# Performance work log

Hardware: AMD Instinct MI355X
Metric: run time of the kernel (lower is better)

Reference implementation:

```python
import jax, jax.numpy as jnp
import numpy as np

H = 8          # num_heads
SCALE = 25.0   # attention temperature
THRESH = 0.75  # raw cosine-similarity mask threshold


def _l2n(x):
    return x / jnp.linalg.norm(x, axis=-1, keepdims=True)


def setup_inputs() -> dict:
    key = jax.random.key(0)
    ks = jax.random.split(key, 8)
    B, N, C, OUT = 1, 2048, 1024, 1024
    s = 0.02
    return {
        "x_cls": jax.random.normal(ks[0], (B, N, C), jnp.float32),
        "x_reg": jax.random.normal(ks[1], (B, N, C), jnp.float32),
        "cls_score": jax.random.uniform(ks[2], (N,), jnp.float32),
        "fg_score": jax.random.uniform(ks[3], (N,), jnp.float32),
        "W_qkv_cls": jax.random.normal(ks[4], (3 * C, C), jnp.float32) * s,
        "W_qkv_reg": jax.random.normal(ks[5], (3 * C, C), jnp.float32) * s,
        "W1": jax.random.normal(ks[6], (2 * C, 2 * C), jnp.float32) * s,
        "b1": jnp.zeros((2 * C,), jnp.float32),
        "W2": jax.random.normal(ks[7], (OUT, 4 * C), jnp.float32) * s,
        "b2": jnp.zeros((OUT,), jnp.float32),
    }


def reference(x_cls, x_reg, cls_score, fg_score, W_qkv_cls, W_qkv_reg, W1, b1, W2, b2):
    B, N, C = x_cls.shape
    d = C // H

    def split_qkv(x, W):
        # nn.Linear (no bias): x @ W.T, then [B,N,3,H,d] -> [3,B,H,N,d]
        qkv = (x @ W.T).reshape(B, N, 3, H, d).transpose(2, 0, 3, 1, 4)
        return qkv[0], qkv[1], qkv[2]

    q_cls, k_cls, v_cls = split_qkv(x_cls, W_qkv_cls)
    q_reg, k_reg, _ = split_qkv(x_reg, W_qkv_reg)

    q_cls, k_cls = _l2n(q_cls), _l2n(k_cls)
    q_reg, k_reg = _l2n(q_reg), _l2n(k_reg)
    v_cls_n = _l2n(v_cls)

    cs = cls_score.reshape(1, 1, 1, N)  # broadcast over [B,H,N,N]
    fs = fg_score.reshape(1, 1, 1, N)

    attn_cls_raw = jnp.einsum('bhnd,bhmd->bhnm', v_cls_n, v_cls_n)
    attn_cls = jax.nn.softmax(jnp.einsum('bhnd,bhmd->bhnm', q_cls, k_cls) * SCALE * cs, axis=-1)
    attn_reg = jax.nn.softmax(jnp.einsum('bhnd,bhmd->bhnm', q_reg, k_reg) * SCALE * fs, axis=-1)
    attn = (attn_reg + attn_cls) * 0.5

    x = jnp.einsum('bhnm,bhmd->bhnd', attn, v_cls).transpose(0, 2, 1, 3).reshape(B, N, C)
    x_ori = v_cls.transpose(0, 2, 1, 3).reshape(B, N, C)
    trans_cls = jnp.concatenate([x, x_ori], axis=-1)  # [B,N,2C]

    # head-averaged similarity, masked and re-normalized (batch element 0)
    sim_raw = attn_cls_raw.sum(axis=1)[0] / H          # [N,N]
    sim_mask = (sim_raw > THRESH).astype(x_cls.dtype)
    sim_attn = attn.sum(axis=1)[0] / H
    sim_round2 = jax.nn.softmax(sim_attn, axis=-1)
    masked = sim_mask * sim_round2
    sim_round2 = masked / masked.sum(axis=-1, keepdims=True)

    msa = trans_cls @ W1.T + b1                        # linear1 [B,N,2C]
    feat = msa[0]                                      # [N,2C]
    soft_sim = sim_round2 @ feat                       # [N,2C]
    ave = jnp.concatenate([soft_sim, feat], axis=-1)   # [N,4C]
    out = ave @ W2.T + b2                              # [N,OUT]
    return out
```

## Files before the change

### kernel.cpp

```cpp
#include <hip/hip_runtime.h>
#include <math.h>

#define PN 2048
#define PC 1024
#define PH 8
#define PD 128
#define PC3 3072

typedef __bf16 bf16x8 __attribute__((ext_vector_type(8)));
typedef float  f32x4  __attribute__((ext_vector_type(4)));
typedef short  s8v    __attribute__((ext_vector_type(8)));
typedef short  s4v    __attribute__((ext_vector_type(4)));

__device__ __forceinline__ short f2bf(float x) {
    unsigned u = __float_as_uint(x);
    unsigned r = (u + 0x7fffu + ((u >> 16) & 1u)) >> 16;
    return (short)r;
}
__device__ __forceinline__ float bf2f(short s) {
    return __uint_as_float(((unsigned)(unsigned short)s) << 16);
}

#define LDS_DMA(g, l) __builtin_amdgcn_global_load_lds( \
    (const __attribute__((address_space(1))) void*)(g), \
    (__attribute__((address_space(3))) void*)(l), 16, 0, 0)

__device__ __forceinline__ void stage128(const short* g, long ld, short* lds,
                                         int wave, int lrow, int lcol)
{
#pragma unroll
    for (int kc = 0; kc < 4; ++kc) {
        LDS_DMA(g + (long)lrow * ld + kc * 32 + lcol, lds + kc * 4096 + wave * 512);
        LDS_DMA(g + (long)(lrow + 64) * ld + kc * 32 + lcol,
                lds + kc * 4096 + 2048 + wave * 512);
    }
}

template<int BN, bool OBF16, bool BIAS>
__global__ __launch_bounds__(256) void mfma_gemm_k(
    const short* __restrict__ A, int lda, long zsa,
    const short* __restrict__ B, int ldb, long zsb,
    void* __restrict__ Cv, int ldc, long zsc,
    int K, float alpha, const float* __restrict__ bias)
{
    constexpr int NJ = BN / 32;
    __shared__ short As[128 * 32];
    __shared__ short Bs[BN * 32];
    const int tid = threadIdx.x;
    const int wave = tid >> 6, lane = tid & 63;
    const int lrow = tid >> 2;
    const int lcol = (tid & 3) * 8;
    const int z = blockIdx.z;
    A += (long)z * zsa;
    B += (long)z * zsb;
    const int row0 = blockIdx.y * 128, col0 = blockIdx.x * BN;
    const short* Ag = A + (long)(row0 + lrow) * lda + lcol;
    const short* Bg = B + (long)(col0 + lrow) * ldb + lcol;
    short* AsW0 = As + wave * 512;
    short* AsW1 = As + 2048 + wave * 512;
    short* BsW0 = Bs + wave * 512;
    short* BsW1 = Bs + 2048 + wave * 512;
    const int wr = (wave >> 1) * 64, wc = (wave & 1) * (BN / 2);
    const int m16 = lane & 15, q8 = (lane >> 4) * 8;

    f32x4 acc[4][NJ];
#pragma unroll
    for (int i = 0; i < 4; ++i)
#pragma unroll
        for (int j = 0; j < NJ; ++j) acc[i][j] = (f32x4){0.f, 0.f, 0.f, 0.f};

    for (int kt = 0; kt < K; kt += 32) {
        if (kt) __syncthreads();
        LDS_DMA(Ag + kt, AsW0);
        LDS_DMA(Ag + kt + 64 * (long)lda, AsW1);
        LDS_DMA(Bg + kt, BsW0);
        if (BN == 128) LDS_DMA(Bg + kt + 64 * (long)ldb, BsW1);
        __syncthreads();
        bf16x8 a[4], b[NJ];
#pragma unroll
        for (int i = 0; i < 4; ++i)
            a[i] = *(const bf16x8*)&As[(wr + i * 16 + m16) * 32 + q8];
#pragma unroll
        for (int j = 0; j < NJ; ++j)
            b[j] = *(const bf16x8*)&Bs[(wc + j * 16 + m16) * 32 + q8];
#pragma unroll
        for (int i = 0; i < 4; ++i)
#pragma unroll
            for (int j = 0; j < NJ; ++j)
                acc[i][j] = __builtin_amdgcn_mfma_f32_16x16x32_bf16(a[i], b[j], acc[i][j], 0, 0, 0);
    }

    const long cz = (long)z * zsc;
#pragma unroll
    for (int i = 0; i < 4; ++i) {
        const int r0 = row0 + wr + i * 16 + (lane >> 4) * 4;
#pragma unroll
        for (int j = 0; j < NJ; ++j) {
            const int c = col0 + wc + j * 16 + m16;
            const float bv = BIAS ? bias[c] : 0.0f;
#pragma unroll
            for (int t = 0; t < 4; ++t) {
                const float x = acc[i][j][t] * alpha + bv;
                const long off = cz + (long)(r0 + t) * ldc + c;
                if (OBF16) ((short*)Cv)[off] = f2bf(x);
                else       ((float*)Cv)[off] = x;
            }
        }
    }
}

__global__ __launch_bounds__(256) void attn_rowsum_k(
    const short* __restrict__ qkv,
    const float* __restrict__ cls_score, const float* __restrict__ fg_score,
    float* __restrict__ l_g)
{
    __shared__ short Qs[16384];
    __shared__ short Ks[16384];
    __shared__ float lsum[128][2];
    const int tid = threadIdx.x, wave = tid >> 6, lane = tid & 63;
    const int lrow = tid >> 2, lcol = (tid & 3) * 8;
    const int wr = (wave >> 1) * 64, wc = (wave & 1) * 64;
    const int m16 = lane & 15, q4 = lane >> 4, q8 = q4 * 8;
    const int row0 = blockIdx.x * 128, h = blockIdx.y, side = blockIdx.z;
    const float* sc_g = side ? fg_score : cls_score;
    const short* base = qkv + (long)side * PN * PC3 + h * PD;
    const short* Kg = base + PC;
    stage128(base + (long)row0 * PC3, PC3, Qs, wave, lrow, lcol);
    stage128(Kg, PC3, Ks, wave, lrow, lcol);
    __syncthreads();
    bf16x8 a[4][4];
#pragma unroll
    for (int i = 0; i < 4; ++i)
#pragma unroll
        for (int kc = 0; kc < 4; ++kc)
            a[i][kc] = *(const bf16x8*)&Qs[kc * 4096 + (wr + i * 16 + m16) * 32 + q8];
    float rs[4][4] = {};
    for (int ct = 0; ct < 16; ++ct) {
        if (ct) {
            __syncthreads();
            stage128(Kg + (long)ct * 128 * PC3, PC3, Ks, wave, lrow, lcol);
            __syncthreads();
        }
        f32x4 acc[4][4];
#pragma unroll
        for (int i = 0; i < 4; ++i)
#pragma unroll
            for (int j = 0; j < 4; ++j) acc[i][j] = (f32x4){0.f, 0.f, 0.f, 0.f};
#pragma unroll
        for (int kc = 0; kc < 4; ++kc) {
            bf16x8 b[4];
#pragma unroll
            for (int j = 0; j < 4; ++j)
                b[j] = *(const bf16x8*)&Ks[kc * 4096 + (wc + j * 16 + m16) * 32 + q8];
#pragma unroll
            for (int i = 0; i < 4; ++i)
#pragma unroll
                for (int j = 0; j < 4; ++j)
                    acc[i][j] = __builtin_amdgcn_mfma_f32_16x16x32_bf16(a[i][kc], b[j], acc[i][j], 0, 0, 0);
        }
#pragma unroll
        for (int j = 0; j < 4; ++j) {
            const float s25 = 25.0f * sc_g[ct * 128 + wc + j * 16 + m16];
#pragma unroll
            for (int i = 0; i < 4; ++i)
#pragma unroll
                for (int t = 0; t < 4; ++t)
                    rs[i][t] += __expf(acc[i][j][t] * s25);
        }
    }
#pragma unroll
    for (int i = 0; i < 4; ++i)
#pragma unroll
        for (int t = 0; t < 4; ++t) {
            float v = rs[i][t];
            v += __shfl_xor(v, 1, 64); v += __shfl_xor(v, 2, 64);
            v += __shfl_xor(v, 4, 64); v += __shfl_xor(v, 8, 64);
            if (m16 == 0) lsum[wr + i * 16 + q4 * 4 + t][wave & 1] = v;
        }
    __syncthreads();
    if (tid < 128)
        l_g[((long)side * PH + h) * PN + row0 + tid] = lsum[tid][0] + lsum[tid][1];
}

__global__ __launch_bounds__(256) void attn_combine_k(
    const short* __restrict__ qkv,
    const float* __restrict__ cls_score, const float* __restrict__ fg_score,
    const float* __restrict__ l_g,
    short* __restrict__ attn8, float* __restrict__ sim_attn)
{
    __shared__ short Ts[32768];
    const int tid = threadIdx.x, wave = tid >> 6, lane = tid & 63;
    const int lrow = tid >> 2, lcol = (tid & 3) * 8;
    const int wr = (wave >> 1) * 64, wc = (wave & 1) * 64;
    const int m16 = lane & 15, q4 = lane >> 4, q8 = q4 * 8;
    const int col0 = blockIdx.x * 128, row0 = blockIdx.y * 128;
    const long NN = (long)PN * PN;

    f32x4 sim[4][4];
#pragma unroll
    for (int i = 0; i < 4; ++i)
#pragma unroll
        for (int j = 0; j < 4; ++j) sim[i][j] = (f32x4){0.f, 0.f, 0.f, 0.f};
    f32x4 comb[4][4];

    for (int st = 0; st < 16; ++st) {
        const int h = st >> 1, s = st & 1;
        const short* bq = qkv + (long)s * PN * PC3 + h * PD;
        __syncthreads();
        stage128(bq + (long)row0 * PC3, PC3, Ts, wave, lrow, lcol);
        stage128(bq + PC + (long)col0 * PC3, PC3, Ts + 16384, wave, lrow, lcol);
        __syncthreads();

        float rl[4];
#pragma unroll
        for (int j = 0; j < 4; ++j)
            rl[j] = 0.5f / l_g[((long)s * PH + h) * PN + row0 + wr + j * 16 + m16];

        f32x4 acc[4][4];
#pragma unroll
        for (int i = 0; i < 4; ++i)
#pragma unroll
            for (int j = 0; j < 4; ++j) acc[i][j] = (f32x4){0.f, 0.f, 0.f, 0.f};
#pragma unroll
        for (int kc = 0; kc < 4; ++kc) {
            bf16x8 kf[4], qf[4];
#pragma unroll
            for (int i = 0; i < 4; ++i)
                kf[i] = *(const bf16x8*)&Ts[16384 + kc * 4096 + (wc + i * 16 + m16) * 32 + q8];
#pragma unroll
            for (int j = 0; j < 4; ++j)
                qf[j] = *(const bf16x8*)&Ts[kc * 4096 + (wr + j * 16 + m16) * 32 + q8];
#pragma unroll
            for (int i = 0; i < 4; ++i)
#pragma unroll
                for (int j = 0; j < 4; ++j)
                    acc[i][j] = __builtin_amdgcn_mfma_f32_16x16x32_bf16(kf[i], qf[j], acc[i][j], 0, 0, 0);
        }
        const float* sc_g = s ? fg_score : cls_score;
#pragma unroll
        for (int i = 0; i < 4; ++i) {
            const f32x4 sc4 = *(const f32x4*)&sc_g[col0 + wc + i * 16 + q4 * 4];
#pragma unroll
            for (int j = 0; j < 4; ++j)
#pragma unroll
                for (int t = 0; t < 4; ++t) {
                    const float e = __expf(acc[i][j][t] * (25.0f * sc4[t])) * rl[j];
                    comb[i][j][t] = s ? (comb[i][j][t] + e) : e;
                }
        }
        if (s) {
#pragma unroll
            for (int j = 0; j < 4; ++j) {
                const long rb = (long)h * NN + (long)(row0 + wr + j * 16 + m16) * PN
                              + col0 + wc + q4 * 4;
#pragma unroll
                for (int i = 0; i < 4; ++i) {
                    s4v o;
#pragma unroll
                    for (int t = 0; t < 4; ++t) o[t] = f2bf(comb[i][j][t]);
                    *(s4v*)&attn8[rb + i * 16] = o;
                    sim[i][j] += comb[i][j] * 0.125f;
                }
            }
        }
    }
#pragma unroll
    for (int j = 0; j < 4; ++j) {
        const long rb = (long)(row0 + wr + j * 16 + m16) * PN + col0 + wc + q4 * 4;
#pragma unroll
        for (int i = 0; i < 4; ++i)
            *(f32x4*)&sim_attn[rb + i * 16] = sim[i][j];
    }
}

__global__ __launch_bounds__(256) void f2bf6_k(
    const float* __restrict__ s0, const float* __restrict__ s1,
    const float* __restrict__ s2, const float* __restrict__ s3,
    const float* __restrict__ s4, const float* __restrict__ s5,
    short* __restrict__ dst)
{
    const int n0 = 512 * 1024, n1 = 512 * 1024, n2 = 768 * 1024,
              n3 = 768 * 1024, n4 = 1024 * 1024;
    const int i = blockIdx.x * 256 + threadIdx.x;
    const float* src;
    int j = i;
    if (j < n0) src = s0;
    else { j -= n0; if (j < n1) src = s1;
    else { j -= n1; if (j < n2) src = s2;
    else { j -= n2; if (j < n3) src = s3;
    else { j -= n3; if (j < n4) src = s4;
    else { j -= n4; src = s5; } } } } }
    float4 v = ((const float4*)src)[j];
    s4v o;
    o[0] = f2bf(v.x); o[1] = f2bf(v.y); o[2] = f2bf(v.z); o[3] = f2bf(v.w);
    ((s4v*)dst)[i] = o;
}

__global__ __launch_bounds__(256) void transpose_bf16_k(
    const short* __restrict__ src, int sld, short* __restrict__ dst, int dld)
{
    __shared__ short tl[64][72];
    const int r0 = blockIdx.y * 64, c0 = blockIdx.x * 64;
    const int tr = threadIdx.x >> 2;
    const int tc = (threadIdx.x & 3) * 16;
    const short* sp = src + (long)(r0 + tr) * sld + c0 + tc;
    s8v v0 = *(const s8v*)sp;
    s8v v1 = *(const s8v*)(sp + 8);
    *(s8v*)&tl[tr][tc] = v0;
    *(s8v*)&tl[tr][tc + 8] = v1;
    __syncthreads();
    s8v o0, o1;
#pragma unroll
    for (int k = 0; k < 8; ++k) { o0[k] = tl[tc + k][tr]; o1[k] = tl[tc + 8 + k][tr]; }
    short* dp = dst + (long)(c0 + tr) * dld + r0 + tc;
    *(s8v*)dp = o0;
    *(s8v*)(dp + 8) = o1;
}

__global__ __launch_bounds__(256) void norms_k(short* __restrict__ qkv,
                                               short* __restrict__ Vn,
                                               short* __restrict__ trans)
{
    const int n = blockIdx.x, which = blockIdx.y, t = threadIdx.x;
    if (which < 4) {
        short* p = qkv + (long)(which >> 1) * ((long)PN * PC3)
                 + (long)n * PC3 + (which & 1) * PC + t * 4;
        s4v v = *(s4v*)p;
        float f0 = bf2f(v[0]), f1 = bf2f(v[1]), f2 = bf2f(v[2]), f3 = bf2f(v[3]);
        float ss = f0 * f0 + f1 * f1 + f2 * f2 + f3 * f3;
        ss += __shfl_xor(ss, 16, 64); ss += __shfl_xor(ss, 8, 64);
        ss += __shfl_xor(ss, 4, 64);  ss += __shfl_xor(ss, 2, 64);
        ss += __shfl_xor(ss, 1, 64);
        const float rn = rsqrtf(ss);
        s4v o;
        o[0] = f2bf(f0 * rn); o[1] = f2bf(f1 * rn);
        o[2] = f2bf(f2 * rn); o[3] = f2bf(f3 * rn);
        *(s4v*)p = o;
    } else {
        const short* p = qkv + (long)n * PC3 + 2 * PC + t * 4;
        s4v v = *(const s4v*)p;
        float f0 = bf2f(v[0]), f1 = bf2f(v[1]), f2 = bf2f(v[2]), f3 = bf2f(v[3]);
        float ss = f0 * f0 + f1 * f1 + f2 * f2 + f3 * f3;
        ss += __shfl_xor(ss, 16, 64); ss += __shfl_xor(ss, 8, 64);
        ss += __shfl_xor(ss, 4, 64);  ss += __shfl_xor(ss, 2, 64);
        ss += __shfl_xor(ss, 1, 64);
        const float rn = rsqrtf(ss);
        s4v o;
        o[0] = f2bf(f0 * rn); o[1] = f2bf(f1 * rn);
        o[2] = f2bf(f2 * rn); o[3] = f2bf(f3 * rn);
        *(s4v*)(Vn + (long)n * PC + t * 4) = o;
        *(s4v*)(trans + (long)n * (2 * PC) + PC + t * 4) = v;
    }
}

__device__ __forceinline__ float wave_sum(float v) {
#pragma unroll
    for (int o = 32; o > 0; o >>= 1) v += __shfl_xor(v, o, 64);
    return v;
}
__device__ __forceinline__ float wave_max(float v) {
#pragma unroll
    for (int o = 32; o > 0; o >>= 1) v = fmaxf(v, __shfl_xor(v, o, 64));
    return v;
}
__device__ __forceinline__ float block_sum(float v, float* sm) {
    v = wave_sum(v);
    __syncthreads();
    if ((threadIdx.x & 63) == 0) sm[threadIdx.x >> 6] = v;
    __syncthreads();
    return sm[0] + sm[1] + sm[2] + sm[3];
}
__device__ __forceinline__ float block_max(float v, float* sm) {
    v = wave_max(v);
    __syncthreads();
    if ((threadIdx.x & 63) == 0) sm[threadIdx.x >> 6] = v;
    __syncthreads();
    return fmaxf(fmaxf(sm[0], sm[1]), fmaxf(sm[2], sm[3]));
}

__global__ __launch_bounds__(256) void sim_round2_k(
    const float* __restrict__ S, const short* __restrict__ Sraw,
    short* __restrict__ Sout)
{
    __shared__ float sm[4];
    const long row = (long)blockIdx.x * PN;
    const int t = threadIdx.x;
    float v[8];
    bool keep[8];
#pragma unroll
    for (int j = 0; j < 8; ++j) {
        const int m = t + 256 * j;
        v[j] = S[row + m];
        keep[j] = bf2f(Sraw[row + m]) > 0.75f;
    }
    float mx = -1e30f;
#pragma unroll
    for (int j = 0; j < 8; ++j) mx = fmaxf(mx, v[j]);
    mx = block_max(mx, sm);
    float sum = 0.f;
#pragma unroll
    for (int j = 0; j < 8; ++j) { v[j] = __expf(v[j] - mx); sum += v[j]; }
    sum = block_sum(sum, sm);
    const float inv = 1.0f / sum;
    float msum = 0.f;
#pragma unroll
    for (int j = 0; j < 8; ++j) { v[j] = keep[j] ? v[j] * inv : 0.f; msum += v[j]; }
    msum = block_sum(msum, sm);
    const float minv = 1.0f / msum;
#pragma unroll
    for (int j = 0; j < 8; ++j) {
        const int m = t + 256 * j;
        Sout[row + m] = f2bf(v[j] * minv);
    }
}

extern "C" void kernel_launch(void* const* d_in, const int* in_sizes, int n_in,
                              void* d_out, int out_size, void* d_ws, size_t ws_size,
                              hipStream_t stream)
{
    (void)in_sizes; (void)n_in; (void)out_size; (void)ws_size;
    const float* x_cls = (const float*)d_in[0];
    const float* x_reg = (const float*)d_in[1];
    const float* cls_score = (const float*)d_in[2];
    const float* fg_score = (const float*)d_in[3];
    const float* Wqc = (const float*)d_in[4];
    const float* Wqr = (const float*)d_in[5];
    const float* W1 = (const float*)d_in[6];
    const float* b1 = (const float*)d_in[7];
    const float* W2 = (const float*)d_in[8];
    const float* b2 = (const float*)d_in[9];
    float* out = (float*)d_out;

    char* w = (char*)d_ws;
    short* qkv_cls_bf = (short*)(w + ((size_t)0   << 20));
    short* qkv_reg_bf = (short*)(w + ((size_t)12  << 20));
    short* attn8      = (short*)(w + ((size_t)24  << 20));
    float* sim_attn   = (float*)(w + ((size_t)88  << 20));
    short* sim_raw_bf = (short*)(w + ((size_t)104 << 20));
    short* Vn         = (short*)(w + ((size_t)112 << 20));
    short* vT         = (short*)(w + ((size_t)116 << 20));
    short* bf_all     = (short*)(w + ((size_t)120 << 20));
    short* x_cls_bf   = bf_all;
    short* x_reg_bf   = (short*)(w + ((size_t)124 << 20));
    short* Wqc_bf     = (short*)(w + ((size_t)128 << 20));
    short* Wqr_bf     = (short*)(w + ((size_t)134 << 20));
    short* W1_bf      = (short*)(w + ((size_t)140 << 20));
    short* W2_bf      = (short*)(w + ((size_t)148 << 20));
    float* l_g        = (float*)(w + ((size_t)156 << 20));
    short* trans      = (short*)(w + ((size_t)120 << 20));
    short* sim_bf     = (short*)(w + ((size_t)24  << 20));
    short* featT      = (short*)(w + ((size_t)32  << 20));
    short* ave        = (short*)(w + ((size_t)40  << 20));

    const long NN = (long)PN * PN;

    f2bf6_k<<<18432, 256, 0, stream>>>(x_cls, x_reg, Wqc, Wqr, W1, W2, bf_all);

    mfma_gemm_k<128, true, false><<<dim3(24, 16, 1), 256, 0, stream>>>(
        x_cls_bf, PC, 0, Wqc_bf, PC, 0, qkv_cls_bf, PC3, 0, PC, 1.0f, nullptr);
    mfma_gemm_k<128, true, false><<<dim3(16, 16, 1), 256, 0, stream>>>(
        x_reg_bf, PC, 0, Wqr_bf, PC, 0, qkv_reg_bf, PC3, 0, PC, 1.0f, nullptr);

    norms_k<<<dim3(PN, 5), 256, 0, stream>>>(qkv_cls_bf, Vn, trans);
    transpose_bf16_k<<<dim3(PC / 64, PN / 64), 256, 0, stream>>>(
        qkv_cls_bf + 2 * PC, PC3, vT, PN);

    mfma_gemm_k<128, true, false><<<dim3(16, 16, 1), 256, 0, stream>>>(
        Vn, PC, 0, Vn, PC, 0, sim_raw_bf, PN, 0, PC, 0.125f, nullptr);

    attn_rowsum_k<<<dim3(16, PH, 2), 256, 0, stream>>>(
        qkv_cls_bf, cls_score, fg_score, l_g);
    attn_combine_k<<<dim3(16, 16), 256, 0, stream>>>(
        qkv_cls_bf, cls_score, fg_score, l_g, attn8, sim_attn);

    mfma_gemm_k<64, true, false><<<dim3(2, 16, PH), 256, 0, stream>>>(
        attn8, PN, NN, vT, PN, (long)PD * PN, trans, 2 * PC, PD, PN, 1.0f, nullptr);

    sim_round2_k<<<PN, 256, 0, stream>>>(sim_attn, sim_raw_bf, sim_bf);

    mfma_gemm_k<128, true, true><<<dim3(16, 16, 1), 256, 0, stream>>>(
        trans, 2 * PC, 0, W1_bf, 2 * PC, 0, ave + 2 * PC, 4 * PC, 0, 2 * PC, 1.0f, b1);

    transpose_bf16_k<<<dim3(32, 32), 256, 0, stream>>>(ave + 2 * PC, 4 * PC, featT, 2 * PC);

    mfma_gemm_k<128, true, false><<<dim3(16, 16, 1), 256, 0, stream>>>(
        sim_bf, 2 * PC, 0, featT, 2 * PC, 0, ave, 4 * PC, 0, 2 * PC, 1.0f, nullptr);

    mfma_gemm_k<64, false, true><<<dim3(16, 16, 1), 256, 0, stream>>>(
        ave, 4 * PC, 0, W2_bf, 4 * PC, 0, out, PC, 0, 4 * PC, 1.0f, b2);
}
```

Baseline: 504.1 us.

## Split attention rowsum and combine kernels across heads and key chunks for more blocks

The rowsum kernel now splits the key dimension into four chunks per block and accumulates partial softmax denominators with atomicAdd into a zeroed buffer. The combine kernel gets one block per head instead of looping over all eight heads, which raises the grid from 256 to 2048 blocks. The fp32 head-averaged sim_attn matrix is no longer written; sim_round2 recomputes it by summing the eight bf16 attention maps with vectorized loads. This trades more parallelism and less fp32 traffic for extra bf16 reads, slightly lower precision in the head average, and a memset plus atomics.

```diff
diff --git a/kernel.cpp b/kernel.cpp
--- a/kernel.cpp
+++ b/kernel.cpp
@@ -121,12 +121,13 @@
     const int lrow = tid >> 2, lcol = (tid & 3) * 8;
     const int wr = (wave >> 1) * 64, wc = (wave & 1) * 64;
     const int m16 = lane & 15, q4 = lane >> 4, q8 = q4 * 8;
-    const int row0 = blockIdx.x * 128, h = blockIdx.y, side = blockIdx.z;
+    const int row0 = blockIdx.x * 128, h = blockIdx.y;
+    const int side = blockIdx.z >> 2, chunk = blockIdx.z & 3;
     const float* sc_g = side ? fg_score : cls_score;
     const short* base = qkv + (long)side * PN * PC3 + h * PD;
     const short* Kg = base + PC;
     stage128(base + (long)row0 * PC3, PC3, Qs, wave, lrow, lcol);
-    stage128(Kg, PC3, Ks, wave, lrow, lcol);
+    stage128(Kg + (long)chunk * 4 * 128 * PC3, PC3, Ks, wave, lrow, lcol);
     __syncthreads();
     bf16x8 a[4][4];
 #pragma unroll
@@ -135,10 +136,11 @@
         for (int kc = 0; kc < 4; ++kc)
             a[i][kc] = *(const bf16x8*)&Qs[kc * 4096 + (wr + i * 16 + m16) * 32 + q8];
     float rs[4][4] = {};
-    for (int ct = 0; ct < 16; ++ct) {
+    for (int ct = 0; ct < 4; ++ct) {
+        const int ctg = chunk * 4 + ct;
         if (ct) {
             __syncthreads();
-            stage128(Kg + (long)ct * 128 * PC3, PC3, Ks, wave, lrow, lcol);
+            stage128(Kg + (long)ctg * 128 * PC3, PC3, Ks, wave, lrow, lcol);
             __syncthreads();
         }
         f32x4 acc[4][4];
@@ -160,7 +162,7 @@
         }
 #pragma unroll
         for (int j = 0; j < 4; ++j) {
-            const float s25 = 25.0f * sc_g[ct * 128 + wc + j * 16 + m16];
+            const float s25 = 25.0f * sc_g[ctg * 128 + wc + j * 16 + m16];
 #pragma unroll
             for (int i = 0; i < 4; ++i)
 #pragma unroll
@@ -179,32 +181,28 @@
         }
     __syncthreads();
     if (tid < 128)
-        l_g[((long)side * PH + h) * PN + row0 + tid] = lsum[tid][0] + lsum[tid][1];
+        atomicAdd(&l_g[((long)side * PH + h) * PN + row0 + tid],
+                  lsum[tid][0] + lsum[tid][1]);
 }
 
 __global__ __launch_bounds__(256) void attn_combine_k(
     const short* __restrict__ qkv,
     const float* __restrict__ cls_score, const float* __restrict__ fg_score,
     const float* __restrict__ l_g,
-    short* __restrict__ attn8, float* __restrict__ sim_attn)
+    short* __restrict__ attn8)
 {
     __shared__ short Ts[32768];
     const int tid = threadIdx.x, wave = tid >> 6, lane = tid & 63;
     const int lrow = tid >> 2, lcol = (tid & 3) * 8;
     const int wr = (wave >> 1) * 64, wc = (wave & 1) * 64;
     const int m16 = lane & 15, q4 = lane >> 4, q8 = q4 * 8;
-    const int col0 = blockIdx.x * 128, row0 = blockIdx.y * 128;
+    const int col0 = blockIdx.x * 128, row0 = blockIdx.y * 128, h = blockIdx.z;
     const long NN = (long)PN * PN;
 
-    f32x4 sim[4][4];
-#pragma unroll
-    for (int i = 0; i < 4; ++i)
-#pragma unroll
-        for (int j = 0; j < 4; ++j) sim[i][j] = (f32x4){0.f, 0.f, 0.f, 0.f};
     f32x4 comb[4][4];
 
-    for (int st = 0; st < 16; ++st) {
-        const int h = st >> 1, s = st & 1;
+#pragma unroll
+    for (int s = 0; s < 2; ++s) {
         const short* bq = qkv + (long)s * PN * PC3 + h * PD;
         __syncthreads();
         stage128(bq + (long)row0 * PC3, PC3, Ts, wave, lrow, lcol);
@@ -248,28 +246,18 @@
                     comb[i][j][t] = s ? (comb[i][j][t] + e) : e;
                 }
         }
-        if (s) {
-#pragma unroll
-            for (int j = 0; j < 4; ++j) {
-                const long rb = (long)h * NN + (long)(row0 + wr + j * 16 + m16) * PN
-                              + col0 + wc + q4 * 4;
-#pragma unroll
-                for (int i = 0; i < 4; ++i) {
-                    s4v o;
-#pragma unroll
-                    for (int t = 0; t < 4; ++t) o[t] = f2bf(comb[i][j][t]);
-                    *(s4v*)&attn8[rb + i * 16] = o;
-                    sim[i][j] += comb[i][j] * 0.125f;
-                }
-            }
-        }
     }
 #pragma unroll
     for (int j = 0; j < 4; ++j) {
-        const long rb = (long)(row0 + wr + j * 16 + m16) * PN + col0 + wc + q4 * 4;
-#pragma unroll
-        for (int i = 0; i < 4; ++i)
-            *(f32x4*)&sim_attn[rb + i * 16] = sim[i][j];
+        const long rb = (long)h * NN + (long)(row0 + wr + j * 16 + m16) * PN
+                      + col0 + wc + q4 * 4;
+#pragma unroll
+        for (int i = 0; i < 4; ++i) {
+            s4v o;
+#pragma unroll
+            for (int t = 0; t < 4; ++t) o[t] = f2bf(comb[i][j][t]);
+            *(s4v*)&attn8[rb + i * 16] = o;
+        }
     }
 }
 
@@ -379,19 +367,27 @@
 }
 
 __global__ __launch_bounds__(256) void sim_round2_k(
-    const float* __restrict__ S, const short* __restrict__ Sraw,
+    const short* __restrict__ attn8, const short* __restrict__ Sraw,
     short* __restrict__ Sout)
 {
     __shared__ float sm[4];
-    const long row = (long)blockIdx.x * PN;
-    const int t = threadIdx.x;
-    float v[8];
+    const long NN = (long)PN * PN;
+    const long rowoff = (long)blockIdx.x * PN + threadIdx.x * 8;
+    float v[8] = {0.f, 0.f, 0.f, 0.f, 0.f, 0.f, 0.f, 0.f};
+#pragma unroll
+    for (int h = 0; h < PH; ++h) {
+        s8v a = *(const s8v*)&attn8[(long)h * NN + rowoff];
+#pragma unroll
+        for (int j = 0; j < 8; ++j) v[j] += bf2f(a[j]);
+    }
     bool keep[8];
-#pragma unroll
-    for (int j = 0; j < 8; ++j) {
-        const int m = t + 256 * j;
-        v[j] = S[row + m];
-        keep[j] = bf2f(Sraw[row + m]) > 0.75f;
+    {
+        s8v raw = *(const s8v*)&Sraw[rowoff];
+#pragma unroll
+        for (int j = 0; j < 8; ++j) {
+            v[j] *= 0.125f;
+            keep[j] = bf2f(raw[j]) > 0.75f;
+        }
     }
     float mx = -1e30f;
 #pragma unroll
@@ -407,11 +403,10 @@
     for (int j = 0; j < 8; ++j) { v[j] = keep[j] ? v[j] * inv : 0.f; msum += v[j]; }
     msum = block_sum(msum, sm);
     const float minv = 1.0f / msum;
-#pragma unroll
-    for (int j = 0; j < 8; ++j) {
-        const int m = t + 256 * j;
-        Sout[row + m] = f2bf(v[j] * minv);
-    }
+    s8v o;
+#pragma unroll
+    for (int j = 0; j < 8; ++j) o[j] = f2bf(v[j] * minv);
+    *(s8v*)&Sout[rowoff] = o;
 }
 
 extern "C" void kernel_launch(void* const* d_in, const int* in_sizes, int n_in,
@@ -435,7 +430,7 @@
     short* qkv_cls_bf = (short*)(w + ((size_t)0   << 20));
     short* qkv_reg_bf = (short*)(w + ((size_t)12  << 20));
     short* attn8      = (short*)(w + ((size_t)24  << 20));
-    float* sim_attn   = (float*)(w + ((size_t)88  << 20));
+    short* sim_bf     = (short*)(w + ((size_t)88  << 20));
     short* sim_raw_bf = (short*)(w + ((size_t)104 << 20));
     short* Vn         = (short*)(w + ((size_t)112 << 20));
     short* vT         = (short*)(w + ((size_t)116 << 20));
@@ -448,7 +443,6 @@
     short* W2_bf      = (short*)(w + ((size_t)148 << 20));
     float* l_g        = (float*)(w + ((size_t)156 << 20));
     short* trans      = (short*)(w + ((size_t)120 << 20));
-    short* sim_bf     = (short*)(w + ((size_t)24  << 20));
     short* featT      = (short*)(w + ((size_t)32  << 20));
     short* ave        = (short*)(w + ((size_t)40  << 20));
 
@@ -468,15 +462,16 @@
     mfma_gemm_k<128, true, false><<<dim3(16, 16, 1), 256, 0, stream>>>(
         Vn, PC, 0, Vn, PC, 0, sim_raw_bf, PN, 0, PC, 0.125f, nullptr);
 
-    attn_rowsum_k<<<dim3(16, PH, 2), 256, 0, stream>>>(
+    hipMemsetAsync(l_g, 0, (size_t)2 * PH * PN * sizeof(float), stream);
+    attn_rowsum_k<<<dim3(16, PH, 8), 256, 0, stream>>>(
         qkv_cls_bf, cls_score, fg_score, l_g);
-    attn_combine_k<<<dim3(16, 16), 256, 0, stream>>>(
-        qkv_cls_bf, cls_score, fg_score, l_g, attn8, sim_attn);
+    attn_combine_k<<<dim3(16, 16, PH), 256, 0, stream>>>(
+        qkv_cls_bf, cls_score, fg_score, l_g, attn8);
 
     mfma_gemm_k<64, true, false><<<dim3(2, 16, PH), 256, 0, stream>>>(
         attn8, PN, NN, vT, PN, (long)PD * PN, trans, 2 * PC, PD, PN, 1.0f, nullptr);
 
-    sim_round2_k<<<PN, 256, 0, stream>>>(sim_attn, sim_raw_bf, sim_bf);
+    sim_round2_k<<<PN, 256, 0, stream>>>(attn8, sim_raw_bf, sim_bf);
 
     mfma_gemm_k<128, true, true><<<dim3(16, 16, 1), 256, 0, stream>>>(
         trans, 2 * PC, 0, W1_bf, 2 * PC, 0, ave + 2 * PC, 4 * PC, 0, 2 * PC, 1.0f, b1);
```

After: 514.8 us. +2.1%, slower.
